# Kernel tuning notes

Measured on AMD Instinct MI355X. Metric: run time of the kernel, lower is better.

## Reference

```python
import jax, jax.numpy as jnp
import numpy as np

BIG = 1e10


def setup_inputs() -> dict:
    key = jax.random.key(0)
    k1, k2, k3, k4 = jax.random.split(key, 4)
    B, N = 8, 4096
    pred = jax.random.normal(k1, (B, N, 3), dtype=jnp.float32)
    target = jax.random.normal(k2, (B, N, 3), dtype=jnp.float32)
    points = jax.random.normal(k3, (B, N, 3), dtype=jnp.float32)
    mask = jax.random.randint(k4, (B, N), 0, 2, dtype=jnp.int32)
    return {"pred": pred, "target": target, "mask": mask, "points": points}


def reference(pred, target, mask, points):
    # clean / predicted point clouds: points plus residual displacements
    clean = points + target          # [B, N, 3]
    predp = points + pred            # [B, N, 3]
    m = mask.astype(bool)            # [B, N] validity mask (same mask for both sets)

    # (avoids materializing a [B, N, N, 3] difference tensor).
    x2 = jnp.sum(clean * clean, axis=-1)                    # [B, N]
    y2 = jnp.sum(predp * predp, axis=-1)                    # [B, N]
    xy = jnp.einsum('bnd,bmd->bnm', clean, predp)           # [B, N, N]
    d = jnp.maximum(x2[:, :, None] + y2[:, None, :] - 2.0 * xy, 0.0)  # [B, N, N]

    # For each clean point (row), nearest valid pred point: mask invalid columns.
    min_x = jnp.min(jnp.where(m[:, None, :], d, BIG), axis=2)  # [B, N]
    # For each pred point (col), nearest valid clean point: mask invalid rows.
    min_y = jnp.min(jnp.where(m[:, :, None], d, BIG), axis=1)  # [B, N]

    cnt = jnp.sum(m, axis=1).astype(jnp.float32)                # valid points per sample
    cham_x = jnp.sum(jnp.where(m, min_x, 0.0), axis=1) / cnt    # point_reduction='mean'
    cham_y = jnp.sum(jnp.where(m, min_y, 0.0), axis=1) / cnt

    # batch_reduction='sum' across samples, then divide by number of batches
    B = mask.shape[0]
    return jnp.sum(cham_x + cham_y) / B
```

## Files before the change

kernel.cpp:

```cpp
#include <hip/hip_runtime.h>

#define NPTS 4096
#define BATCH 8
#define BIGF 1e10f

typedef __attribute__((ext_vector_type(8))) short short8;
typedef __attribute__((ext_vector_type(16))) float f32x16;
typedef unsigned short us;

__device__ __forceinline__ us f2bf(float f) {
    unsigned u = __float_as_uint(f);
    return (us)((u + 0x7FFFu + ((u >> 16) & 1u)) >> 16);
}
__device__ __forceinline__ float bff(us s) { return __uint_as_float(((unsigned)s) << 16); }
__device__ __forceinline__ void split2(float v, us* h, us* m) {
    *h = f2bf(v); *m = f2bf(v - bff(*h));
}
__device__ __forceinline__ unsigned pk2(us a, us b) { return (unsigned)a | ((unsigned)b << 16); }

__device__ __forceinline__ void apackA(float x, float y, float z,
                                       uint4* __restrict__ dst, int row) {
    const us one = 0x3F80;
    us thx,tmx, thy,tmy, thz,tmz, x2h,x2m;
    split2(-2.f*x, &thx,&tmx);
    split2(-2.f*y, &thy,&tmy);
    split2(-2.f*z, &thz,&tmz);
    split2(x*x + y*y + z*z, &x2h,&x2m);
    dst[row]      = make_uint4(pk2(thx,thy), pk2(thz,thx), pk2(thy,thz), pk2(tmx,tmy));
    dst[row + 32] = make_uint4(pk2(tmz,x2h), pk2(x2m,one), pk2(one,0),   pk2(0,0));
}

__device__ __forceinline__ void bpackB(
    const float* __restrict__ points, const float* __restrict__ bres,
    const int* __restrict__ mask, int g, uint4* __restrict__ dst, int col)
{
    float x = points[g*3+0] + bres[g*3+0];
    float y = points[g*3+1] + bres[g*3+1];
    float z = points[g*3+2] + bres[g*3+2];
    float wq = x*x + y*y + z*z + (mask[g] ? 0.f : BIGF);
    const us one = 0x3F80;
    us bhx,bmx, bhy,bmy, bhz,bmz, wh,wm;
    split2(x, &bhx,&bmx);
    split2(y, &bhy,&bmy);
    split2(z, &bhz,&bmz);
    split2(wq, &wh,&wm);
    dst[col]      = make_uint4(pk2(bhx,bhy), pk2(bhz,bmx), pk2(bmy,bmz), pk2(bhx,bhy));
    dst[col + 32] = make_uint4(pk2(bhz,one), pk2(one,wh),  pk2(wm,0),    pk2(0,0));
}

__global__ __launch_bounds__(512, 2) void fused_kernel(
    const float* __restrict__ pred, const float* __restrict__ target,
    const int* __restrict__ mask, const float* __restrict__ points,
    float* __restrict__ out)
{
    __shared__ uint4 Bsh[2][16][64];
    __shared__ uint4 Ash[8][64];
    __shared__ float scnt[8], swave[8];

    int bid = blockIdx.x;
    int strip = bid & 15, b = (bid >> 4) & 7, dir = bid >> 7;
    int t = threadIdx.x, w = t >> 6, lane = t & 63;

    const float* __restrict__ ares = dir ? pred : target;
    const float* __restrict__ bres = dir ? target : pred;

    if (t < 256) {
        int g = b * NPTS + strip * 256 + t;
        float x = points[g*3+0] + ares[g*3+0];
        float y = points[g*3+1] + ares[g*3+1];
        float z = points[g*3+2] + ares[g*3+2];
        apackA(x, y, z, &Ash[t >> 5][0], t & 31);
    }
    bpackB(points, bres, mask, b * NPTS + t, &Bsh[0][t >> 5][0], t & 31);

    int csum = 0;
    const int4* m4 = (const int4*)(mask + b * NPTS);
#pragma unroll
    for (int r = 0; r < 2; r++) { int4 v = m4[r * 512 + t]; csum += v.x + v.y + v.z + v.w; }
#pragma unroll
    for (int s = 32; s; s >>= 1) csum += __shfl_down(csum, s, 64);
    if (lane == 0) scnt[w] = (float)csum;

    float rm[16];
#pragma unroll
    for (int r = 0; r < 16; r++) rm[r] = 3e38f;
    f32x16 zero = {0.f,0.f,0.f,0.f,0.f,0.f,0.f,0.f,0.f,0.f,0.f,0.f,0.f,0.f,0.f,0.f};

    __syncthreads();

    short8 Af = ((const short8*)Ash)[w * 64 + lane];

    for (int c = 0; c < 8; c++) {
        int nb = c & 1;
        if (c < 7)
            bpackB(points, bres, mask, b * NPTS + (c + 1) * 512 + t,
                   &Bsh[nb ^ 1][t >> 5][0], t & 31);
        const short8* Bt = (const short8*)&Bsh[nb][0][0];
#pragma unroll
        for (int p = 0; p < 16; p += 2) {
            short8 b0 = Bt[(p + 0) * 64 + lane];
            short8 b1 = Bt[(p + 1) * 64 + lane];
            f32x16 d0 = __builtin_amdgcn_mfma_f32_32x32x16_bf16(Af, b0, zero, 0, 0, 0);
            f32x16 d1 = __builtin_amdgcn_mfma_f32_32x32x16_bf16(Af, b1, zero, 0, 0, 0);
#pragma unroll
            for (int r = 0; r < 16; r++)
                rm[r] = fminf(fminf(rm[r], d0[r]), d1[r]);
        }
        __syncthreads();
    }

#pragma unroll
    for (int r = 0; r < 16; r++) {
#pragma unroll
        for (int s = 1; s <= 16; s <<= 1)
            rm[r] = fminf(rm[r], __shfl_xor(rm[r], s, 64));
    }
    float part = 0.f;
    if ((lane & 31) == 0) {
        int h = lane >> 5;
        int rowbase = b * NPTS + strip * 256 + w * 32 + 4 * h;
#pragma unroll
        for (int r = 0; r < 16; r++) {
            int row = rowbase + (r & 3) + 8 * (r >> 2);
            if (mask[row]) part += fmaxf(rm[r], 0.f);
        }
    }
    part += __shfl_xor(part, 32, 64);
    if (lane == 0) swave[w] = part;
    __syncthreads();
    if (t == 0) {
        float C = 0.f, S = 0.f;
#pragma unroll
        for (int i = 0; i < 8; i++) { C += scnt[i]; S += swave[i]; }
        atomicAdd(out, S / C * 0.125f);
    }
}

extern "C" void kernel_launch(void* const* d_in, const int* in_sizes, int n_in,
                              void* d_out, int out_size, void* d_ws, size_t ws_size,
                              hipStream_t stream) {
    const float* pred   = (const float*)d_in[0];
    const float* target = (const float*)d_in[1];
    const int*   mask   = (const int*)d_in[2];
    const float* points = (const float*)d_in[3];
    float* out = (float*)d_out;

    hipMemsetAsync(out, 0, sizeof(float), stream);
    fused_kernel<<<256, 512, 0, stream>>>(pred, target, mask, points, out);
}
```

Baseline: 26.35 us.

## Give each wave two A tiles over half the B columns to reuse B fragments

Each wave now holds two 32-row A fragments and covers only half of each B chunk's 16 column tiles, so every B fragment read from LDS feeds two MFMAs instead of one. This halves LDS B reads per MFMA. The two column halves' row minima are combined through a new shared-memory buffer and an extra barrier before the masked sum. The doubled accumulator registers led to dropping the min-2-blocks launch bound hint, which may lower occupancy.

```diff
diff --git a/kernel.cpp b/kernel.cpp
--- a/kernel.cpp
+++ b/kernel.cpp
@@ -48,18 +48,21 @@
     dst[col + 32] = make_uint4(pk2(bhz,one), pk2(one,wh),  pk2(wm,0),    pk2(0,0));
 }
 
-__global__ __launch_bounds__(512, 2) void fused_kernel(
+__global__ __launch_bounds__(512) void fused_kernel(
     const float* __restrict__ pred, const float* __restrict__ target,
     const int* __restrict__ mask, const float* __restrict__ points,
     float* __restrict__ out)
 {
     __shared__ uint4 Bsh[2][16][64];
     __shared__ uint4 Ash[8][64];
+    __shared__ float smin[256][2];
     __shared__ float scnt[8], swave[8];
 
     int bid = blockIdx.x;
     int strip = bid & 15, b = (bid >> 4) & 7, dir = bid >> 7;
     int t = threadIdx.x, w = t >> 6, lane = t & 63;
+    int wq = w & 3;
+    int wh = w >> 2;
 
     const float* __restrict__ ares = dir ? pred : target;
     const float* __restrict__ bres = dir ? target : pred;
@@ -81,30 +84,36 @@
     for (int s = 32; s; s >>= 1) csum += __shfl_down(csum, s, 64);
     if (lane == 0) scnt[w] = (float)csum;
 
-    float rm[16];
+    float rm0[16], rm1[16];
 #pragma unroll
-    for (int r = 0; r < 16; r++) rm[r] = 3e38f;
+    for (int r = 0; r < 16; r++) { rm0[r] = 3e38f; rm1[r] = 3e38f; }
     f32x16 zero = {0.f,0.f,0.f,0.f,0.f,0.f,0.f,0.f,0.f,0.f,0.f,0.f,0.f,0.f,0.f,0.f};
 
     __syncthreads();
 
-    short8 Af = ((const short8*)Ash)[w * 64 + lane];
+    short8 Af0 = ((const short8*)Ash)[(2 * wq + 0) * 64 + lane];
+    short8 Af1 = ((const short8*)Ash)[(2 * wq + 1) * 64 + lane];
 
     for (int c = 0; c < 8; c++) {
         int nb = c & 1;
         if (c < 7)
             bpackB(points, bres, mask, b * NPTS + (c + 1) * 512 + t,
                    &Bsh[nb ^ 1][t >> 5][0], t & 31);
-        const short8* Bt = (const short8*)&Bsh[nb][0][0];
+        const short8* Bt = (const short8*)&Bsh[nb][wh * 8][0];
 #pragma unroll
-        for (int p = 0; p < 16; p += 2) {
+        for (int p = 0; p < 8; p += 2) {
             short8 b0 = Bt[(p + 0) * 64 + lane];
             short8 b1 = Bt[(p + 1) * 64 + lane];
-            f32x16 d0 = __builtin_amdgcn_mfma_f32_32x32x16_bf16(Af, b0, zero, 0, 0, 0);
-            f32x16 d1 = __builtin_amdgcn_mfma_f32_32x32x16_bf16(Af, b1, zero, 0, 0, 0);
+            f32x16 d00 = __builtin_amdgcn_mfma_f32_32x32x16_bf16(Af0, b0, zero, 0, 0, 0);
+            f32x16 d01 = __builtin_amdgcn_mfma_f32_32x32x16_bf16(Af0, b1, zero, 0, 0, 0);
 #pragma unroll
             for (int r = 0; r < 16; r++)
-                rm[r] = fminf(fminf(rm[r], d0[r]), d1[r]);
+                rm0[r] = fminf(fminf(rm0[r], d00[r]), d01[r]);
+            f32x16 d10 = __builtin_amdgcn_mfma_f32_32x32x16_bf16(Af1, b0, zero, 0, 0, 0);
+            f32x16 d11 = __builtin_amdgcn_mfma_f32_32x32x16_bf16(Af1, b1, zero, 0, 0, 0);
+#pragma unroll
+            for (int r = 0; r < 16; r++)
+                rm1[r] = fminf(fminf(rm1[r], d10[r]), d11[r]);
         }
         __syncthreads();
     }
@@ -112,20 +121,30 @@
 #pragma unroll
     for (int r = 0; r < 16; r++) {
 #pragma unroll
-        for (int s = 1; s <= 16; s <<= 1)
-            rm[r] = fminf(rm[r], __shfl_xor(rm[r], s, 64));
+        for (int s = 1; s <= 16; s <<= 1) {
+            rm0[r] = fminf(rm0[r], __shfl_xor(rm0[r], s, 64));
+            rm1[r] = fminf(rm1[r], __shfl_xor(rm1[r], s, 64));
+        }
     }
-    float part = 0.f;
     if ((lane & 31) == 0) {
         int h = lane >> 5;
-        int rowbase = b * NPTS + strip * 256 + w * 32 + 4 * h;
+        int base = wq * 64 + 4 * h;
 #pragma unroll
         for (int r = 0; r < 16; r++) {
-            int row = rowbase + (r & 3) + 8 * (r >> 2);
-            if (mask[row]) part += fmaxf(rm[r], 0.f);
+            int rr = (r & 3) + 8 * (r >> 2);
+            smin[base + rr][wh]      = rm0[r];
+            smin[base + 32 + rr][wh] = rm1[r];
         }
     }
-    part += __shfl_xor(part, 32, 64);
+    __syncthreads();
+
+    float part = 0.f;
+    if (t < 256) {
+        float m = fminf(smin[t][0], smin[t][1]);
+        if (mask[b * NPTS + strip * 256 + t]) part = fmaxf(m, 0.f);
+    }
+#pragma unroll
+    for (int s = 32; s; s >>= 1) part += __shfl_down(part, s, 64);
     if (lane == 0) swave[w] = part;
     __syncthreads();
     if (t == 0) {
```

Result: slower. 27.18 us (+3.2%).
